# Optimization experiments

Hardware: AMD Instinct MI355X
Metric: run time of the kernel (lower is better)

Reference implementation:

```python
import jax, jax.numpy as jnp
import numpy as np

BATCH_SIZE = 4096
TEMPERATURE = 0.5
DIAG_NEG = -50000.0
EPS = 1e-8  # torch CosineSimilarity eps


def setup_inputs() -> dict:
    key = jax.random.key(0)
    k1, k2 = jax.random.split(key)
    z_i = jax.random.normal(k1, (BATCH_SIZE, 128), dtype=jnp.float32)
    z_j = jax.random.normal(k2, (BATCH_SIZE, 128), dtype=jnp.float32)
    return {"z_i": z_i, "z_j": z_j}


def reference(z_i, z_j):
    n = z_i.shape[0]
    z = jnp.concatenate([z_i, z_j], axis=0)  # [2N, D]
    # cosine similarity: normalize once, then one GEMM (same math as
    # CosineSimilarity(dim=2) on the broadcasted pair, with eps clamp on norms)
    norms = jnp.maximum(jnp.linalg.norm(z, axis=-1, keepdims=True), EPS)
    zn = z / norms
    sim = (zn @ zn.T) / TEMPERATURE  # [2N, 2N]
    # mask self-similarity on the diagonal
    idx = jnp.arange(2 * n)
    sim = sim.at[idx, idx].set(DIAG_NEG)
    # labels: positive pair is the other view
    labels = jnp.concatenate([idx[n:], idx[:n]])  # [2N]
    # mean softmax cross-entropy
    logp = jax.nn.log_softmax(sim, axis=-1)
    loss = -jnp.mean(logp[idx, labels])
    return loss
```

## Files before the change

### kernel.cpp

```cpp
#include <hip/hip_runtime.h>

#define N2 8192
#define NHALF 4096
#define DDIM 128
#define NCHUNK 16
#define CPC 512
#define NT 8
#define LN2F 0.69314718055994530942f
#define SCALEF 1.6986436f

typedef __attribute__((ext_vector_type(8))) short bf8_t;
typedef __attribute__((ext_vector_type(4))) float f4_t;

__device__ __forceinline__ float fexp2(float x) { return __builtin_amdgcn_exp2f(x); }
__device__ __forceinline__ float flog2(float x) { return __builtin_amdgcn_logf(x); }

__device__ __forceinline__ unsigned short f2bf(float f) {
  unsigned int x = __float_as_uint(f);
  x += 0x7fffu + ((x >> 16) & 1u);
  return (unsigned short)(x >> 16);
}
__device__ __forceinline__ float bf2f(unsigned short h) {
  return __uint_as_float(((unsigned int)h) << 16);
}

__global__ __launch_bounds__(256) void knorm(const float* __restrict__ zi,
                                             const float* __restrict__ zj,
                                             unsigned short* __restrict__ u,
                                             float* __restrict__ dhat) {
  const int lane = threadIdx.x & 63;
  const int row = blockIdx.x * 4 + (threadIdx.x >> 6);
  const float* src = (row < NHALF) ? (zi + (size_t)row * DDIM)
                                   : (zj + (size_t)(row - NHALF) * DDIM);
  float2 x = *(const float2*)(src + lane * 2);
  float ss = x.x * x.x + x.y * x.y;
#pragma unroll
  for (int m = 32; m; m >>= 1) ss += __shfl_xor(ss, m);
  float scale = SCALEF / fmaxf(sqrtf(ss), 1e-8f);
  unsigned short b0 = f2bf(x.x * scale);
  unsigned short b1 = f2bf(x.y * scale);
  *(unsigned int*)(u + (size_t)row * DDIM + lane * 2) =
      (unsigned int)b0 | ((unsigned int)b1 << 16);
  float f0 = bf2f(b0), f1 = bf2f(b1);
  float dd = f0 * f0 + f1 * f1;
#pragma unroll
  for (int m = 32; m; m >>= 1) dd += __shfl_xor(dd, m);
  if (lane == 0) dhat[row] = dd;
}

__global__ __launch_bounds__(512) void ksim(const unsigned short* __restrict__ u,
                                            float* __restrict__ Lp) {
  __shared__ short Bls[32768];
  const int tid = threadIdx.x;
  const int lane = tid & 63;
  const int w = tid >> 6;
  const int rb = blockIdx.x >> 4;
  const int chunk = blockIdx.x & 15;
  const int lr = lane & 15, lq = lane >> 4;
  const int rowbase = rb * 256;
  const int colbase = chunk * CPC;

#pragma unroll
  for (int i = 0; i < 8; i++) {
    const int k = w * 8 + i;
    const int row_local = k * 4 + lq;
    const int sdu = lr ^ (4 * (k & 1) + lq);
    const unsigned short* src =
        u + (size_t)(rowbase + row_local) * DDIM + sdu * 8;
    short* dst = &Bls[k * 512];
    __builtin_amdgcn_global_load_lds(
        (const __attribute__((address_space(1))) unsigned int*)src,
        (__attribute__((address_space(3))) unsigned int*)dst, 16, 0, 0);
  }
  asm volatile("s_waitcnt vmcnt(0)" ::: "memory");
  __builtin_amdgcn_sched_barrier(0);
  __builtin_amdgcn_s_barrier();
  __builtin_amdgcn_sched_barrier(0);

  bf8_t a[2][4];
#pragma unroll
  for (int s = 0; s < 2; s++)
#pragma unroll
    for (int kc = 0; kc < 4; kc++) {
      const int R = w * 32 + s * 16 + lr;
      a[s][kc] = *(const bf8_t*)&Bls[(R * 16 + ((kc * 4 + lq) ^ (lr & 7))) * 8];
    }
#pragma unroll
  for (int s = 0; s < 2; s++)
#pragma unroll
    for (int kc = 0; kc < 4; kc++)
      asm volatile("" : "+v"(a[s][kc]));
  __builtin_amdgcn_sched_barrier(0);
  __builtin_amdgcn_s_barrier();
  __builtin_amdgcn_sched_barrier(0);

  f4_t L0 = {0.f, 0.f, 0.f, 0.f}, L1 = {0.f, 0.f, 0.f, 0.f};

  auto STAGE = [&](int t) {
#pragma unroll
    for (int i = 0; i < 2; i++) {
      const int j = w * 2 + i;
      const int col_local = j * 4 + lq;
      const int sdu = lr ^ (4 * (j & 1) + lq);
      const unsigned short* src =
          u + (size_t)(colbase + t * 64 + col_local) * DDIM + sdu * 8;
      short* dst = &Bls[(t % 3) * 8192 + j * 512];
      __builtin_amdgcn_global_load_lds(
          (const __attribute__((address_space(1))) unsigned int*)src,
          (__attribute__((address_space(3))) unsigned int*)dst, 16, 0, 0);
    }
  };

  auto COMP = [&](int t) {
    const short* P = &Bls[(t % 3) * 8192];
#pragma unroll
    for (int g = 0; g < 4; g++) {
      bf8_t bv[4];
#pragma unroll
      for (int kc = 0; kc < 4; kc++)
        bv[kc] = *(const bf8_t*)&P[((g * 16 + lr) * 16 +
                                    ((kc * 4 + lq) ^ (lr & 7))) * 8];
      f4_t acc0 = {0.f, 0.f, 0.f, 0.f}, acc1 = {0.f, 0.f, 0.f, 0.f};
#pragma unroll
      for (int kc = 0; kc < 4; kc++) {
        acc0 = __builtin_amdgcn_mfma_f32_16x16x32_bf16(a[0][kc], bv[kc], acc0, 0, 0, 0);
        acc1 = __builtin_amdgcn_mfma_f32_16x16x32_bf16(a[1][kc], bv[kc], acc1, 0, 0, 0);
      }
#pragma unroll
      for (int r = 0; r < 4; r++) {
        L0[r] += fexp2(acc0[r]);
        L1[r] += fexp2(acc1[r]);
      }
    }
  };

  STAGE(0);
  STAGE(1);
#pragma unroll 1
  for (int t = 0; t < NT; ++t) {
    if (t < NT - 1) {
      asm volatile("s_waitcnt vmcnt(2)" ::: "memory");
    } else {
      asm volatile("s_waitcnt vmcnt(0)" ::: "memory");
    }
    __builtin_amdgcn_sched_barrier(0);
    __builtin_amdgcn_s_barrier();
    __builtin_amdgcn_sched_barrier(0);
    COMP(t);
    if (t + 2 < NT) STAGE(t + 2);
  }

#pragma unroll
  for (int r = 0; r < 4; r++) {
    float v0 = L0[r], v1 = L1[r];
    v0 += __shfl_xor(v0, 1); v0 += __shfl_xor(v0, 2);
    v0 += __shfl_xor(v0, 4); v0 += __shfl_xor(v0, 8);
    v1 += __shfl_xor(v1, 1); v1 += __shfl_xor(v1, 2);
    v1 += __shfl_xor(v1, 4); v1 += __shfl_xor(v1, 8);
    if (lr == 0) {
      const int rrow = rowbase + w * 32 + lq * 4 + r;
      Lp[(size_t)rrow * NCHUNK + chunk] = v0;
      Lp[(size_t)(rrow + 16) * NCHUNK + chunk] = v1;
    }
  }
}

__global__ __launch_bounds__(256) void krow(const unsigned short* __restrict__ u,
                                            const float* __restrict__ dhat,
                                            const float* __restrict__ Lp,
                                            float* __restrict__ bsum) {
  const int lane = threadIdx.x & 63;
  const int w = threadIdx.x >> 6;
  const int i = blockIdx.x * 4 + w;
  const int j = (i + NHALF) & (N2 - 1);

  const unsigned int av = ((const unsigned int*)(u + (size_t)i * DDIM))[lane];
  const unsigned int bv = ((const unsigned int*)(u + (size_t)j * DDIM))[lane];
  float dot = __uint_as_float(av << 16) * __uint_as_float(bv << 16) +
              __uint_as_float(av & 0xffff0000u) * __uint_as_float(bv & 0xffff0000u);
  float ls = (lane < NCHUNK) ? Lp[(size_t)i * NCHUNK + lane] : 0.f;
#pragma unroll
  for (int m = 32; m; m >>= 1) {
    dot += __shfl_xor(dot, m);
    ls += __shfl_xor(ls, m);
  }
  __shared__ float sred[4];
  if (lane == 0) {
    const float L = ls - fexp2(dhat[i]);
    sred[w] = LN2F * (flog2(L) - dot);
  }
  __syncthreads();
  if (threadIdx.x == 0)
    bsum[blockIdx.x] = sred[0] + sred[1] + sred[2] + sred[3];
}

__global__ void kfinal(const float* __restrict__ bsum, float* __restrict__ out) {
  float v = 0.f;
#pragma unroll
  for (int jj = 0; jj < 32; jj++) v += bsum[threadIdx.x + 64 * jj];
#pragma unroll
  for (int m = 32; m; m >>= 1) v += __shfl_xor(v, m);
  if (threadIdx.x == 0) out[0] = v * (1.0f / N2);
}

extern "C" void kernel_launch(void* const* d_in, const int* in_sizes, int n_in,
                              void* d_out, int out_size, void* d_ws, size_t ws_size,
                              hipStream_t stream) {
  const float* zi = (const float*)d_in[0];
  const float* zj = (const float*)d_in[1];
  char* ws = (char*)d_ws;
  unsigned short* u = (unsigned short*)ws;
  float* dhat = (float*)(ws + (size_t)N2 * DDIM * 2);
  float* Lp = (float*)(ws + (size_t)N2 * DDIM * 2 + (size_t)N2 * 4);
  float* bsum = (float*)(ws + (size_t)N2 * DDIM * 2 + (size_t)N2 * 4 +
                         (size_t)NCHUNK * N2 * 4);
  float* out = (float*)d_out;

  hipLaunchKernelGGL(knorm, dim3(N2 / 4), dim3(256), 0, stream, zi, zj, u, dhat);
  hipLaunchKernelGGL(ksim, dim3((N2 / 256) * NCHUNK), dim3(512), 0, stream, u, Lp);
  hipLaunchKernelGGL(krow, dim3(N2 / 4), dim3(256), 0, stream, u, dhat, Lp, bsum);
  hipLaunchKernelGGL(kfinal, dim3(1), dim3(64), 0, stream, bsum, out);
}
```

Measured before the change: 34.41 us.

## Halve ksim waves and give each wave 64 rows for more B-tile reuse

The similarity kernel now launches 256-thread blocks (4 waves) instead of 512. Each wave holds 64 rows of A in registers instead of 32 and runs 4 MFMA accumulators per B fragment, so every LDS read of B feeds twice as many MFMAs. This cuts LDS read traffic per FLOP. In exchange, register pressure rises (16 A fragments plus 4 accumulators) and each block has fewer waves to hide load and exp latency, which may lower occupancy.

```diff
diff --git a/kernel.cpp b/kernel.cpp
--- a/kernel.cpp
+++ b/kernel.cpp
@@ -48,7 +48,7 @@
   if (lane == 0) dhat[row] = dd;
 }
 
-__global__ __launch_bounds__(512) void ksim(const unsigned short* __restrict__ u,
+__global__ __launch_bounds__(256) void ksim(const unsigned short* __restrict__ u,
                                             float* __restrict__ Lp) {
   __shared__ short Bls[32768];
   const int tid = threadIdx.x;
@@ -61,8 +61,8 @@
   const int colbase = chunk * CPC;
 
 #pragma unroll
-  for (int i = 0; i < 8; i++) {
-    const int k = w * 8 + i;
+  for (int i = 0; i < 16; i++) {
+    const int k = w * 16 + i;
     const int row_local = k * 4 + lq;
     const int sdu = lr ^ (4 * (k & 1) + lq);
     const unsigned short* src =
@@ -77,16 +77,16 @@
   __builtin_amdgcn_s_barrier();
   __builtin_amdgcn_sched_barrier(0);
 
-  bf8_t a[2][4];
-#pragma unroll
-  for (int s = 0; s < 2; s++)
+  bf8_t a[4][4];
+#pragma unroll
+  for (int s = 0; s < 4; s++)
 #pragma unroll
     for (int kc = 0; kc < 4; kc++) {
-      const int R = w * 32 + s * 16 + lr;
+      const int R = w * 64 + s * 16 + lr;
       a[s][kc] = *(const bf8_t*)&Bls[(R * 16 + ((kc * 4 + lq) ^ (lr & 7))) * 8];
     }
 #pragma unroll
-  for (int s = 0; s < 2; s++)
+  for (int s = 0; s < 4; s++)
 #pragma unroll
     for (int kc = 0; kc < 4; kc++)
       asm volatile("" : "+v"(a[s][kc]));
@@ -94,12 +94,14 @@
   __builtin_amdgcn_s_barrier();
   __builtin_amdgcn_sched_barrier(0);
 
-  f4_t L0 = {0.f, 0.f, 0.f, 0.f}, L1 = {0.f, 0.f, 0.f, 0.f};
+  f4_t L[4];
+#pragma unroll
+  for (int s = 0; s < 4; s++) L[s] = (f4_t){0.f, 0.f, 0.f, 0.f};
 
   auto STAGE = [&](int t) {
 #pragma unroll
-    for (int i = 0; i < 2; i++) {
-      const int j = w * 2 + i;
+    for (int i = 0; i < 4; i++) {
+      const int j = w * 4 + i;
       const int col_local = j * 4 + lq;
       const int sdu = lr ^ (4 * (j & 1) + lq);
       const unsigned short* src =
@@ -120,17 +122,18 @@
       for (int kc = 0; kc < 4; kc++)
         bv[kc] = *(const bf8_t*)&P[((g * 16 + lr) * 16 +
                                     ((kc * 4 + lq) ^ (lr & 7))) * 8];
-      f4_t acc0 = {0.f, 0.f, 0.f, 0.f}, acc1 = {0.f, 0.f, 0.f, 0.f};
-#pragma unroll
-      for (int kc = 0; kc < 4; kc++) {
-        acc0 = __builtin_amdgcn_mfma_f32_16x16x32_bf16(a[0][kc], bv[kc], acc0, 0, 0, 0);
-        acc1 = __builtin_amdgcn_mfma_f32_16x16x32_bf16(a[1][kc], bv[kc], acc1, 0, 0, 0);
-      }
-#pragma unroll
-      for (int r = 0; r < 4; r++) {
-        L0[r] += fexp2(acc0[r]);
-        L1[r] += fexp2(acc1[r]);
-      }
+      f4_t acc[4];
+#pragma unroll
+      for (int s = 0; s < 4; s++) acc[s] = (f4_t){0.f, 0.f, 0.f, 0.f};
+#pragma unroll
+      for (int kc = 0; kc < 4; kc++)
+#pragma unroll
+        for (int s = 0; s < 4; s++)
+          acc[s] = __builtin_amdgcn_mfma_f32_16x16x32_bf16(a[s][kc], bv[kc], acc[s], 0, 0, 0);
+#pragma unroll
+      for (int s = 0; s < 4; s++)
+#pragma unroll
+        for (int r = 0; r < 4; r++) L[s][r] += fexp2(acc[s][r]);
     }
   };
 
@@ -139,7 +142,7 @@
 #pragma unroll 1
   for (int t = 0; t < NT; ++t) {
     if (t < NT - 1) {
-      asm volatile("s_waitcnt vmcnt(2)" ::: "memory");
+      asm volatile("s_waitcnt vmcnt(4)" ::: "memory");
     } else {
       asm volatile("s_waitcnt vmcnt(0)" ::: "memory");
     }
@@ -151,18 +154,17 @@
   }
 
 #pragma unroll
-  for (int r = 0; r < 4; r++) {
-    float v0 = L0[r], v1 = L1[r];
-    v0 += __shfl_xor(v0, 1); v0 += __shfl_xor(v0, 2);
-    v0 += __shfl_xor(v0, 4); v0 += __shfl_xor(v0, 8);
-    v1 += __shfl_xor(v1, 1); v1 += __shfl_xor(v1, 2);
-    v1 += __shfl_xor(v1, 4); v1 += __shfl_xor(v1, 8);
-    if (lr == 0) {
-      const int rrow = rowbase + w * 32 + lq * 4 + r;
-      Lp[(size_t)rrow * NCHUNK + chunk] = v0;
-      Lp[(size_t)(rrow + 16) * NCHUNK + chunk] = v1;
-    }
-  }
+  for (int s = 0; s < 4; s++)
+#pragma unroll
+    for (int r = 0; r < 4; r++) {
+      float v = L[s][r];
+      v += __shfl_xor(v, 1); v += __shfl_xor(v, 2);
+      v += __shfl_xor(v, 4); v += __shfl_xor(v, 8);
+      if (lr == 0) {
+        const int rrow = rowbase + w * 64 + s * 16 + lq * 4 + r;
+        Lp[(size_t)rrow * NCHUNK + chunk] = v;
+      }
+    }
 }
 
 __global__ __launch_bounds__(256) void krow(const unsigned short* __restrict__ u,
@@ -217,7 +219,7 @@
   float* out = (float*)d_out;
 
   hipLaunchKernelGGL(knorm, dim3(N2 / 4), dim3(256), 0, stream, zi, zj, u, dhat);
-  hipLaunchKernelGGL(ksim, dim3((N2 / 256) * NCHUNK), dim3(512), 0, stream, u, Lp);
+  hipLaunchKernelGGL(ksim, dim3((N2 / 256) * NCHUNK), dim3(256), 0, stream, u, Lp);
   hipLaunchKernelGGL(krow, dim3(N2 / 4), dim3(256), 0, stream, u, dhat, Lp, bsum);
   hipLaunchKernelGGL(kfinal, dim3(1), dim3(64), 0, stream, bsum, out);
 }
```

Measured after the change: 37.50 us. 9.0% more time.
